# Optimization experiments

Hardware: AMD Instinct MI355X
Metric: run time of the kernel (lower is better)

## Reference

```python
import jax, jax.numpy as jnp
import numpy as np

K = 3  # from init kwarg


def setup_inputs() -> dict:
    key = jax.random.key(0)
    k1, k2 = jax.random.split(key)
    B, N, D = 32, 2048, 128
    features = jax.random.normal(k1, (B, N, D), dtype=jnp.float32)
    strength = jax.random.uniform(k2, (), dtype=jnp.float32)
    return {"features": features, "strength": strength}


def reference(features, strength):
    B, N, D = features.shape
    k = min(K, N - 1)
    x = jax.lax.stop_gradient(features)  # torch uses features.detach() for the mix path

    # pairwise euclidean distance (torch.cdist, p=2): ||a||^2 + ||b||^2 - 2 a.b
    sq = jnp.sum(x * x, axis=-1)                     # (B, N)
    d2 = sq[:, :, None] + sq[:, None, :] - 2.0 * jnp.einsum('bnd,bmd->bnm', x, x)
    dist = jnp.sqrt(jnp.maximum(d2, 0.0))            # (B, N, N)

    # mask self-distance with +1e6 on the diagonal
    eye = jnp.eye(N, dtype=dist.dtype)
    dist = dist + eye[None, :, :] * 1000000.0

    # k smallest -> top_k of negated distances
    _, idx = jax.lax.top_k(-dist, k)                 # idx: (B, N, k)

    # gather neighbor features: gathered[b,n,j] = x[b, idx[b,n,j]]
    gathered = x[jnp.arange(B)[:, None, None], idx]  # (B, N, k, D)
    mix = jnp.mean(gathered, axis=2)                 # (B, N, D)

    s = jnp.clip(strength, 0.0, 1.0)
    return (1.0 - s) * features + s * mix
```

## Files before the change

### kernel.cpp

```cpp
#include <hip/hip_runtime.h>
#include <cfloat>

#define BB 32
#define NN 2048
#define DD 128
#define RM 128
#define CN 64
#define NT (NN / CN)

typedef __attribute__((ext_vector_type(8))) short short8;
typedef __attribute__((ext_vector_type(4))) short short4v;
typedef __attribute__((ext_vector_type(4))) float float4v;

__device__ __forceinline__ unsigned short f2bf(float f) {
    unsigned int u = __builtin_bit_cast(unsigned int, f);
    u += 0x7FFFu + ((u >> 16) & 1u);
    return (unsigned short)(u >> 16);
}

__device__ __forceinline__ unsigned int umn(unsigned int a, unsigned int b) { return a < b ? a : b; }
__device__ __forceinline__ unsigned int umx(unsigned int a, unsigned int b) { return a > b ? a : b; }
#define CSU(a, b) { unsigned int _lo = umn(a, b), _hi = umx(a, b); (a) = _lo; (b) = _hi; }

__device__ __forceinline__ unsigned int umed3(unsigned int a, unsigned int b, unsigned int c) {
    unsigned int d;
    asm("v_med3_u32 %0, %1, %2, %3" : "=v"(d) : "v"(a), "v"(b), "v"(c));
    return d;
}

__device__ __forceinline__ void gl2lds16(const unsigned short* g, unsigned short* l) {
    __builtin_amdgcn_global_load_lds(
        (const __attribute__((address_space(1))) void*)g,
        (__attribute__((address_space(3))) void*)l, 16, 0, 0);
}

__global__ __launch_bounds__(256) void prep_kernel(const float* __restrict__ x,
        unsigned short* __restrict__ xb16, float* __restrict__ sq) {
    int c = blockIdx.x * 256 + threadIdx.x;
    float4 v = *reinterpret_cast<const float4*>(x + (size_t)c * 4);
    short4v pk;
    pk[0] = (short)f2bf(v.x); pk[1] = (short)f2bf(v.y);
    pk[2] = (short)f2bf(v.z); pk[3] = (short)f2bf(v.w);
    *reinterpret_cast<short4v*>(xb16 + (size_t)c * 4) = pk;
    float acc = v.x * v.x + v.y * v.y + v.z * v.z + v.w * v.w;
    acc += __shfl_xor(acc, 1);
    acc += __shfl_xor(acc, 2);
    acc += __shfl_xor(acc, 4);
    acc += __shfl_xor(acc, 8);
    acc += __shfl_xor(acc, 16);
    if ((threadIdx.x & 31) == 0) sq[c >> 5] = acc + 1024.0f;
}

__global__ __launch_bounds__(256) void sq_kernel(const float* __restrict__ x,
                                                 float* __restrict__ sq) {
    int t = blockIdx.x * 256 + threadIdx.x;
    int row = t >> 2;
    int q = t & 3;
    const float4* xp = reinterpret_cast<const float4*>(x + (size_t)row * DD + q * 32);
    float acc = 0.f;
#pragma unroll
    for (int i = 0; i < 8; ++i) {
        float4 v = xp[i];
        acc += v.x * v.x + v.y * v.y + v.z * v.z + v.w * v.w;
    }
    acc += __shfl_xor(acc, 1);
    acc += __shfl_xor(acc, 2);
    if (q == 0) sq[row] = acc + 1024.0f;
}

template<bool PRE>
__global__ __launch_bounds__(256, 2) void knn_kernel(const float* __restrict__ x,
        const unsigned short* __restrict__ xb16g,
        const float* __restrict__ sqv, const float* __restrict__ strength,
        float* __restrict__ out) {
    __shared__ __align__(16) unsigned short btile[4 * CN * DD];
    __shared__ unsigned int cand8[RM * 8];

    const int b = blockIdx.x;
    const int row0 = blockIdx.y * RM;
    const int tid = threadIdx.x;
    const int w = tid >> 6;
    const int lane = tid & 63;
    const int m = lane & 15;
    const int quad = lane >> 4;
    const float* __restrict__ xb = x + (size_t)b * NN * DD;
    const unsigned short* __restrict__ gb = PRE ? xb16g + (size_t)b * NN * DD : nullptr;

    short8 afrag[2][4];
    if constexpr (PRE) {
#pragma unroll
        for (int rg = 0; rg < 2; ++rg)
#pragma unroll
            for (int kc = 0; kc < 4; ++kc)
                afrag[rg][kc] = *reinterpret_cast<const short8*>(
                    gb + (size_t)(row0 + 32 * w + rg * 16 + m) * DD + kc * 32 + quad * 8);
    } else {
#pragma unroll
        for (int rg = 0; rg < 2; ++rg)
#pragma unroll
            for (int kc = 0; kc < 4; ++kc) {
                const float4* src = reinterpret_cast<const float4*>(
                    xb + (size_t)(row0 + 32 * w + rg * 16 + m) * DD + kc * 32 + quad * 8);
                float4 v0 = src[0], v1 = src[1];
                short8 pk;
                pk[0] = (short)f2bf(v0.x); pk[1] = (short)f2bf(v0.y);
                pk[2] = (short)f2bf(v0.z); pk[3] = (short)f2bf(v0.w);
                pk[4] = (short)f2bf(v1.x); pk[5] = (short)f2bf(v1.y);
                pk[6] = (short)f2bf(v1.z); pk[7] = (short)f2bf(v1.w);
                afrag[rg][kc] = pk;
            }
    }

    const unsigned short* gsl[4];
    int ldo[4];
    int str_[4], stc_[4], stp_[4];
#pragma unroll
    for (int l = 0; l < 4; ++l) {
        int f = (l * 4 + w) * 64 + lane;
        int r = f >> 4, p = f & 15;
        int c = p ^ (r & 7);
        str_[l] = r; stc_[l] = c; stp_[l] = p;
        if constexpr (PRE) gsl[l] = gb + (size_t)r * DD + c * 8;
        ldo[l] = (l * 4 + w) * 512;
    }
    int baddr[16];
#pragma unroll
    for (int kc = 0; kc < 4; ++kc)
#pragma unroll
        for (int cc = 0; cc < 4; ++cc)
            baddr[kc * 4 + cc] =
                ((cc * 16 + m) * DD + (((kc * 4 + quad) ^ (m & 7)) * 8)) * 2;
    const float* __restrict__ sqp = sqv + (size_t)b * NN + m;

    if constexpr (PRE) {
#pragma unroll
        for (int l = 0; l < 4; ++l) gl2lds16(gsl[l], btile + ldo[l]);
#pragma unroll
        for (int l = 0; l < 4; ++l) gl2lds16(gsl[l] + (1 << 13), btile + CN * DD + ldo[l]);
    } else {
#pragma unroll
        for (int l = 0; l < 8; ++l) {
            int id = l * 256 + tid;
            int r = id >> 4, c = id & 15, p = c ^ (r & 7);
            const float4* src = reinterpret_cast<const float4*>(xb + (size_t)r * DD + c * 8);
            float4 v0 = src[0], v1 = src[1];
            short8 pk;
            pk[0] = (short)f2bf(v0.x); pk[1] = (short)f2bf(v0.y);
            pk[2] = (short)f2bf(v0.z); pk[3] = (short)f2bf(v0.w);
            pk[4] = (short)f2bf(v1.x); pk[5] = (short)f2bf(v1.y);
            pk[6] = (short)f2bf(v1.z); pk[7] = (short)f2bf(v1.w);
            *reinterpret_cast<short8*>(btile + r * DD + p * 8) = pk;
        }
    }
    float sqb[4];
#pragma unroll
    for (int cc = 0; cc < 4; ++cc) sqb[cc] = sqp[cc * 16];
    __syncthreads();

    unsigned int tk[2][4][4];
#pragma unroll
    for (int rg = 0; rg < 2; ++rg)
#pragma unroll
        for (int i = 0; i < 4; ++i)
#pragma unroll
            for (int q = 0; q < 4; ++q) tk[rg][i][q] = 0xFFFFFFFFu;

#define TILE_SLOT(J)                                                                   \
    {                                                                                  \
        const int ct = ct4 + (J);                                                      \
                       \
        float sqn[4];                                                                  \
        if (ct + 1 < NT) {                                                             \
            _Pragma("unroll")                                                          \
            for (int cc = 0; cc < 4; ++cc)                                             \
                sqn[cc] = sqp[((ct + 1) << 6) + cc * 16];                              \
        }                                                                              \
        asm volatile("" ::: "memory");         \
              \
        if (ct + 2 < NT) {                                                             \
            if constexpr (PRE) {                                                       \
                _Pragma("unroll")                                                      \
                for (int l = 0; l < 4; ++l)                                            \
                    gl2lds16(gsl[l] + ((size_t)(ct + 2) << 13),                        \
                             btile + (((J) + 2) & 3) * CN * DD + ldo[l]);              \
            } else {                                                                   \
                _Pragma("unroll")                                                      \
                for (int l = 0; l < 4; ++l) {                                          \
                    const float4* src = reinterpret_cast<const float4*>(               \
                        xb + (size_t)((ct + 2) * CN + str_[l]) * DD + stc_[l] * 8);    \
                    float4 v0 = src[0], v1 = src[1];                                   \
                    short8 pk;                                                         \
                    pk[0] = (short)f2bf(v0.x); pk[1] = (short)f2bf(v0.y);              \
                    pk[2] = (short)f2bf(v0.z); pk[3] = (short)f2bf(v0.w);              \
                    pk[4] = (short)f2bf(v1.x); pk[5] = (short)f2bf(v1.y);              \
                    pk[6] = (short)f2bf(v1.z); pk[7] = (short)f2bf(v1.w);              \
                    *reinterpret_cast<short8*>(btile + (((J) + 2) & 3) * CN * DD       \
                        + str_[l] * DD + stp_[l] * 8) = pk;                            \
                }                                                                      \
            }                                                                          \
        }                                                                              \
                        \
        float4v acc[2][4];                                                             \
        _Pragma("unroll")                                                              \
        for (int rg = 0; rg < 2; ++rg)                                                 \
            _Pragma("unroll")                                                          \
            for (int cc = 0; cc < 4; ++cc) acc[rg][cc] = (float4v){0.f, 0.f, 0.f, 0.f};\
        _Pragma("unroll")                                                              \
        for (int kc = 0; kc < 4; ++kc) {                                               \
            short8 bfrag[4];                                                           \
            _Pragma("unroll")                                                          \
            for (int cc = 0; cc < 4; ++cc)                                             \
                bfrag[cc] = *reinterpret_cast<const short8*>(                          \
                    reinterpret_cast<const char*>(btile)                               \
                    + (J) * (CN * DD * 2) + baddr[kc * 4 + cc]);                       \
            _Pragma("unroll")                                                          \
            for (int rg = 0; rg < 2; ++rg)                                             \
                _Pragma("unroll")                                                      \
                for (int cc = 0; cc < 4; ++cc)                                         \
                    acc[rg][cc] = __builtin_amdgcn_mfma_f32_16x16x32_bf16(             \
                        afrag[rg][kc], bfrag[cc], acc[rg][cc], 0, 0, 0);               \
        }                                                                              \
                            \
        _Pragma("unroll")                                                              \
        for (int cc = 0; cc < 4; ++cc) {                                               \
            unsigned int col = (unsigned int)(ct * CN + cc * 16 + m);                  \
            _Pragma("unroll")                                                          \
            for (int rg = 0; rg < 2; ++rg)                                             \
                _Pragma("unroll")                                                      \
                for (int reg = 0; reg < 4; ++reg) {                                    \
                    float scb = fmaf(-2.f, acc[rg][cc][reg], sqb[cc]);                 \
                    unsigned int key =                                                 \
                        (__builtin_bit_cast(unsigned int, scb) & 0xFFFFF800u) | col;   \
                    unsigned int t0 = tk[rg][reg][0], t1 = tk[rg][reg][1];             \
                    unsigned int t2 = tk[rg][reg][2], t3 = tk[rg][reg][3];             \
                    tk[rg][reg][0] = umn(t0, key);                                     \
                    tk[rg][reg][1] = umed3(t0, t1, key);                               \
                    tk[rg][reg][2] = umed3(t1, t2, key);                               \
                    tk[rg][reg][3] = umed3(t2, t3, key);                               \
                }                                                                      \
        }                                                                              \
                                                                       \
        if (ct + 1 < NT) {                                                             \
            _Pragma("unroll")                                                          \
            for (int cc = 0; cc < 4; ++cc) sqb[cc] = sqn[cc];                          \
        }                                                                              \
                            \
        if constexpr (PRE) {                                                           \
            if (ct + 2 < NT) {                                                         \
                asm volatile("s_waitcnt vmcnt(4)" ::: "memory");                       \
            } else {                                                                   \
                asm volatile("s_waitcnt vmcnt(0)" ::: "memory");                       \
            }                                                                          \
            __builtin_amdgcn_s_barrier();                                              \
            __builtin_amdgcn_sched_barrier(0);                                         \
        } else {                                                                       \
            __syncthreads();                                                           \
        }                                                                              \
    }

#pragma unroll 1
    for (int ct4 = 0; ct4 < NT; ct4 += 4) {
        TILE_SLOT(0)
        TILE_SLOT(1)
        TILE_SLOT(2)
        TILE_SLOT(3)
    }
#undef TILE_SLOT

#pragma unroll
    for (int rg = 0; rg < 2; ++rg)
#pragma unroll
        for (int reg = 0; reg < 4; ++reg) {
            unsigned int e[8];
#pragma unroll
            for (int j = 0; j < 4; ++j) e[j] = tk[rg][reg][j];
#pragma unroll
            for (int j = 4; j < 8; ++j) e[j] = 0xFFFFFFFFu;
#pragma unroll
            for (int st = 0; st < 4; ++st) {
                int mask = 1 << st;
                unsigned int rv[8];
#pragma unroll
                for (int j = 0; j < 8; ++j)
                    rv[j] = (unsigned int)__shfl_xor((int)e[7 - j], mask, 64);
#pragma unroll
                for (int j = 0; j < 8; ++j) e[j] = umn(e[j], rv[j]);
                CSU(e[0], e[4]); CSU(e[1], e[5]); CSU(e[2], e[6]); CSU(e[3], e[7]);
                CSU(e[0], e[2]); CSU(e[1], e[3]); CSU(e[4], e[6]); CSU(e[5], e[7]);
                CSU(e[0], e[1]); CSU(e[2], e[3]); CSU(e[4], e[5]); CSU(e[6], e[7]);
            }
            if (m == 0) {
                int row = 32 * w + rg * 16 + quad * 4 + reg;
#pragma unroll
                for (int j = 0; j < 8; ++j) cand8[row * 8 + j] = e[j];
            }
        }
    __syncthreads();

    double* refd = reinterpret_cast<double*>(btile);
    int* best3 = reinterpret_cast<int*>(btile) + 2048;

    {
        int r = tid >> 1, h = tid & 1;
        int grow = row0 + r;
        int ci[4];
#pragma unroll
        for (int j = 0; j < 4; ++j) ci[j] = (int)(cand8[r * 8 + h * 4 + j] & 0x7FFu);
        const float* pr = xb + (size_t)grow * DD;
        const float* pc[4];
#pragma unroll
        for (int j = 0; j < 4; ++j) pc[j] = xb + (size_t)ci[j] * DD;
        double a[4] = {0.0, 0.0, 0.0, 0.0};
#pragma unroll 4
        for (int d4 = 0; d4 < 32; ++d4) {
            float4 wv = *reinterpret_cast<const float4*>(pr + d4 * 4);
#pragma unroll
            for (int j = 0; j < 4; ++j) {
                float4 v = *reinterpret_cast<const float4*>(pc[j] + d4 * 4);
                double d;
                d = (double)wv.x - (double)v.x; a[j] += d * d;
                d = (double)wv.y - (double)v.y; a[j] += d * d;
                d = (double)wv.z - (double)v.z; a[j] += d * d;
                d = (double)wv.w - (double)v.w; a[j] += d * d;
            }
        }
#pragma unroll
        for (int j = 0; j < 4; ++j)
            refd[r * 8 + h * 4 + j] = (ci[j] == grow) ? DBL_MAX : a[j];
    }
    __syncthreads();

    if (tid < RM) {
        int r = tid;
        double b0 = DBL_MAX, b1 = DBL_MAX, b2 = DBL_MAX;
        int i0 = 0x7fffffff, i1 = 0x7fffffff, i2 = 0x7fffffff;
        for (int e = 0; e < 8; ++e) {
            double dv = refd[r * 8 + e];
            int ix = (int)(cand8[r * 8 + e] & 0x7FFu);
            if (dv < b2 || (dv == b2 && ix < i2)) {
                b2 = dv; i2 = ix;
                if (b1 > b2 || (b1 == b2 && i1 > i2)) { double td = b1; b1 = b2; b2 = td; int tn = i1; i1 = i2; i2 = tn; }
                if (b0 > b1 || (b0 == b1 && i0 > i1)) { double td = b0; b0 = b1; b1 = td; int tn = i0; i0 = i1; i1 = tn; }
            }
        }
        best3[r * 3 + 0] = i0; best3[r * 3 + 1] = i1; best3[r * 3 + 2] = i2;
    }
    __syncthreads();

    {
        int r = tid >> 1, q = tid & 1;
        float s = fminf(fmaxf(strength[0], 0.f), 1.f);
        const float* pa = xb + (size_t)(row0 + r) * DD + q * 64;
        const float* p1 = xb + (size_t)best3[r * 3 + 0] * DD + q * 64;
        const float* p2 = xb + (size_t)best3[r * 3 + 1] * DD + q * 64;
        const float* p3 = xb + (size_t)best3[r * 3 + 2] * DD + q * 64;
        float* po = out + ((size_t)b * NN + row0 + r) * DD + q * 64;
#pragma unroll
        for (int l = 0; l < 16; ++l) {
            float4 a  = *reinterpret_cast<const float4*>(pa + l * 4);
            float4 v1 = *reinterpret_cast<const float4*>(p1 + l * 4);
            float4 v2 = *reinterpret_cast<const float4*>(p2 + l * 4);
            float4 v3 = *reinterpret_cast<const float4*>(p3 + l * 4);
            float4 o;
            o.x = (1.f - s) * a.x + s * ((v1.x + v2.x + v3.x) / 3.f);
            o.y = (1.f - s) * a.y + s * ((v1.y + v2.y + v3.y) / 3.f);
            o.z = (1.f - s) * a.z + s * ((v1.z + v2.z + v3.z) / 3.f);
            o.w = (1.f - s) * a.w + s * ((v1.w + v2.w + v3.w) / 3.f);
            *reinterpret_cast<float4*>(po + l * 4) = o;
        }
    }
}

extern "C" void kernel_launch(void* const* d_in, const int* in_sizes, int n_in,
                              void* d_out, int out_size, void* d_ws, size_t ws_size,
                              hipStream_t stream) {
    const float* x = (const float*)d_in[0];
    const float* strength = (const float*)d_in[1];
    float* out = (float*)d_out;
    float* sq = (float*)d_ws;
    unsigned short* xb16 = (unsigned short*)((char*)d_ws + 256 * 1024);
    const size_t need = 256 * 1024 + (size_t)BB * NN * DD * sizeof(unsigned short);

    if (ws_size >= need) {
        prep_kernel<<<dim3((BB * NN * DD / 4) / 256), 256, 0, stream>>>(x, xb16, sq);
        knn_kernel<true><<<dim3(BB, NN / RM), 256, 0, stream>>>(x, xb16, sq, strength, out);
    } else {
        sq_kernel<<<dim3((BB * NN * 4) / 256), 256, 0, stream>>>(x, sq);
        knn_kernel<false><<<dim3(BB, NN / RM), 256, 0, stream>>>(x, nullptr, sq, strength, out);
    }
}
```

Before: 196.3 us.

## Software-pipeline MFMA of next tile with top-k selection of previous tile

Restructures the column-tile loop so the MFMA distance product for tile ct runs alongside the top-k insertion for tile ct-1. Two accumulator sets alternate between the two roles. LDS buffering drops from four to three tiles, rotated through runtime pointers, and the +1024 bias on squared norms moves from the prep kernels into the main kernel. The goal is to overlap matrix-core work with the VALU-heavy selection, at the cost of more accumulator registers and per-iteration address recomputation.

```diff
diff --git a/kernel.cpp b/kernel.cpp
--- a/kernel.cpp
+++ b/kernel.cpp
@@ -48,7 +48,7 @@
     acc += __shfl_xor(acc, 4);
     acc += __shfl_xor(acc, 8);
     acc += __shfl_xor(acc, 16);
-    if ((threadIdx.x & 31) == 0) sq[c >> 5] = acc + 1024.0f;
+    if ((threadIdx.x & 31) == 0) sq[c >> 5] = acc;
 }
 
 __global__ __launch_bounds__(256) void sq_kernel(const float* __restrict__ x,
@@ -65,7 +65,7 @@
     }
     acc += __shfl_xor(acc, 1);
     acc += __shfl_xor(acc, 2);
-    if (q == 0) sq[row] = acc + 1024.0f;
+    if (q == 0) sq[row] = acc;
 }
 
 template<bool PRE>
@@ -73,7 +73,7 @@
         const unsigned short* __restrict__ xb16g,
         const float* __restrict__ sqv, const float* __restrict__ strength,
         float* __restrict__ out) {
-    __shared__ __align__(16) unsigned short btile[4 * CN * DD];
+    __shared__ __align__(16) unsigned short btile[3 * CN * DD];
     __shared__ unsigned int cand8[RM * 8];
 
     const int b = blockIdx.x;
@@ -111,32 +111,25 @@
             }
     }
 
-    const unsigned short* gsl[4];
-    int ldo[4];
-    int str_[4], stc_[4], stp_[4];
-#pragma unroll
-    for (int l = 0; l < 4; ++l) {
-        int f = (l * 4 + w) * 64 + lane;
-        int r = f >> 4, p = f & 15;
-        int c = p ^ (r & 7);
-        str_[l] = r; stc_[l] = c; stp_[l] = p;
-        if constexpr (PRE) gsl[l] = gb + (size_t)r * DD + c * 8;
-        ldo[l] = (l * 4 + w) * 512;
-    }
-    int baddr[16];
-#pragma unroll
-    for (int kc = 0; kc < 4; ++kc)
-#pragma unroll
-        for (int cc = 0; cc < 4; ++cc)
-            baddr[kc * 4 + cc] =
-                ((cc * 16 + m) * DD + (((kc * 4 + quad) ^ (m & 7)) * 8)) * 2;
-    const float* __restrict__ sqp = sqv + (size_t)b * NN + m;
+    unsigned short* cur = btile;
+    unsigned short* n1  = btile + CN * DD;
+    unsigned short* n2  = btile + 2 * CN * DD;
 
     if constexpr (PRE) {
 #pragma unroll
-        for (int l = 0; l < 4; ++l) gl2lds16(gsl[l], btile + ldo[l]);
-#pragma unroll
-        for (int l = 0; l < 4; ++l) gl2lds16(gsl[l] + (1 << 13), btile + CN * DD + ldo[l]);
+        for (int l = 0; l < 4; ++l) {
+            int f = (l * 4 + w) * 64 + lane;
+            int r = f >> 4, p = f & 15;
+            int c = p ^ (r & 7);
+            gl2lds16(gb + (size_t)r * DD + c * 8, cur + (l * 4 + w) * 512);
+        }
+#pragma unroll
+        for (int l = 0; l < 4; ++l) {
+            int f = (l * 4 + w) * 64 + lane;
+            int r = f >> 4, p = f & 15;
+            int c = p ^ (r & 7);
+            gl2lds16(gb + (size_t)(CN + r) * DD + c * 8, n1 + (l * 4 + w) * 512);
+        }
     } else {
 #pragma unroll
         for (int l = 0; l < 8; ++l) {
@@ -152,9 +145,10 @@
             *reinterpret_cast<short8*>(btile + r * DD + p * 8) = pk;
         }
     }
-    float sqb[4];
-#pragma unroll
-    for (int cc = 0; cc < 4; ++cc) sqb[cc] = sqp[cc * 16];
+    float sqb0[4], sqb1[4];
+#pragma unroll
+    for (int cc = 0; cc < 4; ++cc)
+        sqb0[cc] = sqv[(size_t)b * NN + cc * 16 + m] + 1024.0f;
     __syncthreads();
 
     unsigned int tk[2][4][4];
@@ -165,70 +159,18 @@
 #pragma unroll
             for (int q = 0; q < 4; ++q) tk[rg][i][q] = 0xFFFFFFFFu;
 
-#define TILE_SLOT(J)                                                                   \
+    float4v acc0[2][4], acc1[2][4];
+
+#define SEL(ACCP, SQBP, CTP)                                                           \
     {                                                                                  \
-        const int ct = ct4 + (J);                                                      \
-                       \
-        float sqn[4];                                                                  \
-        if (ct + 1 < NT) {                                                             \
-            _Pragma("unroll")                                                          \
-            for (int cc = 0; cc < 4; ++cc)                                             \
-                sqn[cc] = sqp[((ct + 1) << 6) + cc * 16];                              \
-        }                                                                              \
-        asm volatile("" ::: "memory");         \
-              \
-        if (ct + 2 < NT) {                                                             \
-            if constexpr (PRE) {                                                       \
-                _Pragma("unroll")                                                      \
-                for (int l = 0; l < 4; ++l)                                            \
-                    gl2lds16(gsl[l] + ((size_t)(ct + 2) << 13),                        \
-                             btile + (((J) + 2) & 3) * CN * DD + ldo[l]);              \
-            } else {                                                                   \
-                _Pragma("unroll")                                                      \
-                for (int l = 0; l < 4; ++l) {                                          \
-                    const float4* src = reinterpret_cast<const float4*>(               \
-                        xb + (size_t)((ct + 2) * CN + str_[l]) * DD + stc_[l] * 8);    \
-                    float4 v0 = src[0], v1 = src[1];                                   \
-                    short8 pk;                                                         \
-                    pk[0] = (short)f2bf(v0.x); pk[1] = (short)f2bf(v0.y);              \
-                    pk[2] = (short)f2bf(v0.z); pk[3] = (short)f2bf(v0.w);              \
-                    pk[4] = (short)f2bf(v1.x); pk[5] = (short)f2bf(v1.y);              \
-                    pk[6] = (short)f2bf(v1.z); pk[7] = (short)f2bf(v1.w);              \
-                    *reinterpret_cast<short8*>(btile + (((J) + 2) & 3) * CN * DD       \
-                        + str_[l] * DD + stp_[l] * 8) = pk;                            \
-                }                                                                      \
-            }                                                                          \
-        }                                                                              \
-                        \
-        float4v acc[2][4];                                                             \
-        _Pragma("unroll")                                                              \
-        for (int rg = 0; rg < 2; ++rg)                                                 \
-            _Pragma("unroll")                                                          \
-            for (int cc = 0; cc < 4; ++cc) acc[rg][cc] = (float4v){0.f, 0.f, 0.f, 0.f};\
-        _Pragma("unroll")                                                              \
-        for (int kc = 0; kc < 4; ++kc) {                                               \
-            short8 bfrag[4];                                                           \
-            _Pragma("unroll")                                                          \
-            for (int cc = 0; cc < 4; ++cc)                                             \
-                bfrag[cc] = *reinterpret_cast<const short8*>(                          \
-                    reinterpret_cast<const char*>(btile)                               \
-                    + (J) * (CN * DD * 2) + baddr[kc * 4 + cc]);                       \
-            _Pragma("unroll")                                                          \
-            for (int rg = 0; rg < 2; ++rg)                                             \
-                _Pragma("unroll")                                                      \
-                for (int cc = 0; cc < 4; ++cc)                                         \
-                    acc[rg][cc] = __builtin_amdgcn_mfma_f32_16x16x32_bf16(             \
-                        afrag[rg][kc], bfrag[cc], acc[rg][cc], 0, 0, 0);               \
-        }                                                                              \
-                            \
         _Pragma("unroll")                                                              \
         for (int cc = 0; cc < 4; ++cc) {                                               \
-            unsigned int col = (unsigned int)(ct * CN + cc * 16 + m);                  \
+            unsigned int col = (unsigned int)((CTP) * CN + cc * 16 + m);               \
             _Pragma("unroll")                                                          \
             for (int rg = 0; rg < 2; ++rg)                                             \
                 _Pragma("unroll")                                                      \
                 for (int reg = 0; reg < 4; ++reg) {                                    \
-                    float scb = fmaf(-2.f, acc[rg][cc][reg], sqb[cc]);                 \
+                    float scb = fmaf(-2.f, ACCP[rg][cc][reg], SQBP[cc]);               \
                     unsigned int key =                                                 \
                         (__builtin_bit_cast(unsigned int, scb) & 0xFFFFF800u) | col;   \
                     unsigned int t0 = tk[rg][reg][0], t1 = tk[rg][reg][1];             \
@@ -239,10 +181,76 @@
                     tk[rg][reg][3] = umed3(t2, t3, key);                               \
                 }                                                                      \
         }                                                                              \
-                                                                       \
+    }
+
+#define STEP(ACC_CUR, ACC_PEN, SQB_PEN, CT, DOSEL)                                     \
+    {                                                                                  \
+        const int ct = (CT);                                                           \
+                       \
+        float sqn[4];                                                                  \
         if (ct + 1 < NT) {                                                             \
             _Pragma("unroll")                                                          \
-            for (int cc = 0; cc < 4; ++cc) sqb[cc] = sqn[cc];                          \
+            for (int cc = 0; cc < 4; ++cc)                                             \
+                sqn[cc] = sqv[(size_t)b * NN + (ct + 1) * CN + cc * 16 + m];           \
+        }                                                                              \
+        asm volatile("" ::: "memory");         \
+                  \
+        if (ct + 2 < NT) {                                                             \
+            int cb = (ct + 2) * CN;                                                    \
+            if constexpr (PRE) {                                                       \
+                _Pragma("unroll")                                                      \
+                for (int l = 0; l < 4; ++l) {                                          \
+                    int f = (l * 4 + w) * 64 + lane;                                   \
+                    int r = f >> 4, p = f & 15;                                        \
+                    int c = p ^ (r & 7);                                               \
+                    gl2lds16(gb + (size_t)(cb + r) * DD + c * 8,                       \
+                             n2 + (l * 4 + w) * 512);                                  \
+                }                                                                      \
+            } else {                                                                   \
+                _Pragma("unroll")                                                      \
+                for (int l = 0; l < 4; ++l) {                                          \
+                    int id = l * 256 + tid;                                            \
+                    int r = id >> 4, c = id & 15, p = c ^ (r & 7);                     \
+                    const float4* src = reinterpret_cast<const float4*>(               \
+                        xb + (size_t)(cb + r) * DD + c * 8);                           \
+                    float4 v0 = src[0], v1 = src[1];                                   \
+                    short8 pk;                                                         \
+                    pk[0] = (short)f2bf(v0.x); pk[1] = (short)f2bf(v0.y);              \
+                    pk[2] = (short)f2bf(v0.z); pk[3] = (short)f2bf(v0.w);              \
+                    pk[4] = (short)f2bf(v1.x); pk[5] = (short)f2bf(v1.y);              \
+                    pk[6] = (short)f2bf(v1.z); pk[7] = (short)f2bf(v1.w);              \
+                    *reinterpret_cast<short8*>(n2 + r * DD + p * 8) = pk;              \
+                }                                                                      \
+            }                                                                          \
+        }                                                                              \
+                \
+        _Pragma("unroll")                                                              \
+        for (int rg = 0; rg < 2; ++rg)                                                 \
+            _Pragma("unroll")                                                          \
+            for (int cc = 0; cc < 4; ++cc)                                             \
+                ACC_CUR[rg][cc] = (float4v){0.f, 0.f, 0.f, 0.f};                       \
+        _Pragma("unroll")                                                              \
+        for (int kc = 0; kc < 4; ++kc) {                                               \
+            short8 bfrag[4];                                                           \
+            _Pragma("unroll")                                                          \
+            for (int cc = 0; cc < 4; ++cc) {                                           \
+                int rl = cc * 16 + m;                                                  \
+                int p = (kc * 4 + quad) ^ (m & 7);                                     \
+                bfrag[cc] = *reinterpret_cast<const short8*>(cur + rl * DD + p * 8);   \
+            }                                                                          \
+            _Pragma("unroll")                                                          \
+            for (int rg = 0; rg < 2; ++rg)                                             \
+                _Pragma("unroll")                                                      \
+                for (int cc = 0; cc < 4; ++cc)                                         \
+                    ACC_CUR[rg][cc] = __builtin_amdgcn_mfma_f32_16x16x32_bf16(         \
+                        afrag[rg][kc], bfrag[cc], ACC_CUR[rg][cc], 0, 0, 0);           \
+        }                                                                              \
+                \
+        if (DOSEL) SEL(ACC_PEN, SQB_PEN, ct - 1)                                       \
+                            \
+        if (ct + 1 < NT) {                                                             \
+            _Pragma("unroll")                                                          \
+            for (int cc = 0; cc < 4; ++cc) SQB_PEN[cc] = sqn[cc] + 1024.0f;            \
         }                                                                              \
                             \
         if constexpr (PRE) {                                                           \
@@ -256,16 +264,18 @@
         } else {                                                                       \
             __syncthreads();                                                           \
         }                                                                              \
+                                                                \
+        unsigned short* t = cur; cur = n1; n1 = n2; n2 = t;                            \
     }
 
 #pragma unroll 1
-    for (int ct4 = 0; ct4 < NT; ct4 += 4) {
-        TILE_SLOT(0)
-        TILE_SLOT(1)
-        TILE_SLOT(2)
-        TILE_SLOT(3)
-    }
-#undef TILE_SLOT
+    for (int ct2 = 0; ct2 < NT; ct2 += 2) {
+        STEP(acc0, acc1, sqb1, ct2, (ct2 > 0))
+        STEP(acc1, acc0, sqb0, ct2 + 1, true)
+    }
+    SEL(acc1, sqb1, NT - 1)
+#undef STEP
+#undef SEL
 
 #pragma unroll
     for (int rg = 0; rg < 2; ++rg)
```

Result: slower. 201.1 us (+2.4%).
